# Kernel optimization log

Hardware: AMD Instinct MI355X
Metric: run time of the kernel (lower is better)

## Reference

```python
import jax, jax.numpy as jnp
import numpy as np
import math

B, S, D, H = 2, 2048, 512, 8
DK = D // H  # 64
NEG_INF = float('-inf')


def setup_inputs() -> dict:
    key = jax.random.key(0)
    ks = jax.random.split(key, 16)
    s = 1.0 / math.sqrt(D)
    return {
        'in_Q': jax.random.normal(ks[0], (B, S, D), jnp.float32),
        'in_K': jax.random.normal(ks[1], (B, S, D), jnp.float32),
        'in_V': jax.random.normal(ks[2], (B, S, D), jnp.float32),
        'row_pad_mask': jax.random.randint(ks[3], (B, S), 0, 2, jnp.int32),
        'col_pad_mask': jax.random.randint(ks[4], (B, S), 0, 2, jnp.int32),
        'W_Q': jax.random.uniform(ks[5], (D, D), jnp.float32, -s, s),
        'b_Q': jax.random.uniform(ks[6], (D,), jnp.float32, -s, s),
        'W_K': jax.random.uniform(ks[7], (D, D), jnp.float32, -s, s),
        'b_K': jax.random.uniform(ks[8], (D,), jnp.float32, -s, s),
        'W_V': jax.random.uniform(ks[9], (D, D), jnp.float32, -s, s),
        'b_V': jax.random.uniform(ks[10], (D,), jnp.float32, -s, s),
        'W_O': jax.random.uniform(ks[11], (D, D), jnp.float32, -s, s),
        'b_O': jax.random.uniform(ks[12], (D,), jnp.float32, -s, s),
    }


def reference(in_Q, in_K, in_V, row_pad_mask, col_pad_mask,
              W_Q, b_Q, W_K, b_K, W_V, b_V, W_O, b_O):
    b, sq, _ = in_Q.shape
    sk = in_K.shape[1]
    # projections (torch Linear: x @ W.T + b)
    Q = in_Q @ W_Q.T + b_Q
    K = in_K @ W_K.T + b_K
    V = in_V @ W_V.T + b_V
    # chunk along feature dim + stack == reshape to heads: [b, h, s, dk]
    Qh = Q.reshape(b, sq, H, DK).transpose(0, 2, 1, 3)
    Kh = K.reshape(b, sk, H, DK).transpose(0, 2, 1, 3)
    Vh = V.reshape(b, sk, H, DK).transpose(0, 2, 1, 3)
    scores = jnp.einsum('bhqd,bhkd->bhqk', Qh, Kh) / math.sqrt(DK)
    # causal mask (additive -inf above diagonal, as in the original)
    causal = jnp.triu(jnp.full((sq, sk), NEG_INF, scores.dtype), k=1)
    scores = scores + causal
    # padding masks: pad masks encode lengths via their row sums
    row_len = row_pad_mask.sum(axis=1)  # [b]
    col_len = col_pad_mask.sum(axis=1)
    row_np = jnp.arange(sq)[None, :] < row_len[:, None]  # [b, sq]
    col_np = jnp.arange(sk)[None, :] < col_len[:, None]  # [b, sk]
    non_pad = (row_np[:, :, None] & col_np[:, None, :])[:, None]  # [b,1,sq,sk]
    scores = jnp.where(non_pad, scores, NEG_INF)
    p = jax.nn.softmax(scores, axis=-1)
    p = jnp.nan_to_num(p)  # fully-masked rows -> 0 (matches torch nan_to_num)
    attn = jnp.einsum('bhqk,bhkd->bhqd', p, Vh)
    Hcat = attn.transpose(0, 2, 1, 3).reshape(b, sq, D)
    return Hcat @ W_O.T + b_O
```

## Files before the change

### kernel.cpp

```cpp
#include <hip/hip_runtime.h>

#define S_LEN 2048
#define D_MODEL 512
#define NHEAD 8
#define BATCH 2

typedef __attribute__((ext_vector_type(8))) short bf16x8;
typedef __attribute__((ext_vector_type(4))) float f32x4;

__device__ __forceinline__ unsigned short f2bf(float f) {
    union { float f; unsigned u; } v; v.f = f;
    unsigned u = v.u + 0x7FFFu + ((v.u >> 16) & 1u);
    return (unsigned short)(u >> 16);
}

__device__ __forceinline__ float ex2(float x) {
    return __builtin_amdgcn_exp2f(x);
}

__device__ __forceinline__ unsigned cvtpk(float lo, float hi) {
    unsigned r;
    asm("v_cvt_pk_bf16_f32 %0, %1, %2" : "=v"(r) : "v"(lo), "v"(hi));
    return r;
}

__device__ __forceinline__ void gl_lds16(const unsigned short* g, unsigned short* l) {
    __builtin_amdgcn_global_load_lds(
        (const __attribute__((address_space(1))) void*)g,
        (__attribute__((address_space(3))) void*)l,
        16, 0, 0);
}

__global__ __launch_bounds__(256) void cvtlens_kernel(
    const float* __restrict__ inQ, const float* __restrict__ inK, const float* __restrict__ inV,
    const float* __restrict__ WQ, const float* __restrict__ WK,
    const float* __restrict__ WV, const float* __restrict__ WO,
    const int* __restrict__ rpm, const int* __restrict__ cpm,
    unsigned short* __restrict__ Xbf, unsigned short* __restrict__ Wbf,
    int* __restrict__ lens)
{
    const int t = threadIdx.x;
    if (blockIdx.x < 2) {
        __shared__ int red[256];
        const int b = blockIdx.x;
        int sr = 0, sc2 = 0;
        for (int i = t; i < S_LEN; i += 256) {
            sr  += rpm[b * S_LEN + i];
            sc2 += cpm[b * S_LEN + i];
        }
        red[t] = sr;
        __syncthreads();
        for (int off = 128; off > 0; off >>= 1) {
            if (t < off) red[t] += red[t + off];
            __syncthreads();
        }
        if (t == 0) lens[b * 2 + 0] = red[0];
        __syncthreads();
        red[t] = sc2;
        __syncthreads();
        for (int off = 128; off > 0; off >>= 1) {
            if (t < off) red[t] += red[t + off];
            __syncthreads();
        }
        if (t == 0) lens[b * 2 + 1] = red[0];
    }

    const int NXC = 786432;
    const int NTOT = 917504;
    const int stride = gridDim.x * 256;
    for (int c = blockIdx.x * 256 + t; c < NTOT; c += stride) {
        if (c < NXC) {
            const int flat = c << 3;
            const int z = flat >> 21;
            const int off = flat & 2097151;
            const float* src = ((z == 0) ? inQ : (z == 1) ? inK : inV) + off;
            float4 a = *(const float4*)src;
            float4 d = *(const float4*)(src + 4);
            unsigned short* w = Xbf + flat;
            w[0] = f2bf(a.x); w[1] = f2bf(a.y); w[2] = f2bf(a.z); w[3] = f2bf(a.w);
            w[4] = f2bf(d.x); w[5] = f2bf(d.y); w[6] = f2bf(d.z); w[7] = f2bf(d.w);
        } else {
            const int wflat = (c - NXC) << 3;
            const int wz = wflat >> 18;
            const int off = wflat & 262143;
            const float* src = ((wz == 0) ? WQ : (wz == 1) ? WK : (wz == 2) ? WV : WO) + off;
            float4 a = *(const float4*)src;
            float4 d = *(const float4*)(src + 4);
            unsigned short* w = Wbf + wflat;
            w[0] = f2bf(a.x); w[1] = f2bf(a.y); w[2] = f2bf(a.z); w[3] = f2bf(a.w);
            w[4] = f2bf(d.x); w[5] = f2bf(d.y); w[6] = f2bf(d.z); w[7] = f2bf(d.w);
        }
    }
}

__global__ __launch_bounds__(256) void proj_gemm(
    const unsigned short* __restrict__ Xbf, const unsigned short* __restrict__ Wbf,
    const float* __restrict__ bQ, const float* __restrict__ bK, const float* __restrict__ bV,
    const int* __restrict__ lens,
    unsigned short* __restrict__ Qg, unsigned short* __restrict__ Kg,
    unsigned short* __restrict__ VTg)
{
    __shared__ __align__(16) unsigned short Xld[2][8192];
    __shared__ __align__(16) unsigned short Wld[2][8192];

    const int z = blockIdx.z;
    const int tileS = blockIdx.x * 128;
    const int tileF = blockIdx.y * 128;
    const int bb0 = tileS >> 11;
    const int rl = lens[bb0 * 2], cl = lens[bb0 * 2 + 1];
    const int limit = (z == 0) ? rl : cl;
    if ((tileS & 2047) >= limit) return;

    const unsigned short* X = Xbf + (size_t)z * (4096 * 512);
    const unsigned short* W = Wbf + (size_t)z * (512 * 512);
    const float* bias = (z == 0) ? bQ : (z == 1) ? bK : bV;

    const int t = threadIdx.x;
    const int wv = t >> 6, lane = t & 63, l15 = lane & 15, quad = lane >> 4;
    const int ro = lane >> 3;
    const int lc8 = ((lane & 7) ^ ro) * 8;

    const unsigned short* gX = X + (size_t)(tileS + wv * 32 + ro) * 512 + lc8;
    const unsigned short* gW = W + (size_t)(tileF + wv * 32 + ro) * 512 + lc8;
    const int wvo = wv * 2048;

    const int f_off = (wv & 1) * 64, s_off = (wv >> 1) * 64;
    const int swk = l15 & 7;

    f32x4 acc[4][4] = {};

    #pragma unroll
    for (int j = 0; j < 4; ++j) {
        gl_lds16(gX + j * 4096, &Xld[0][wvo + j * 512]);
        gl_lds16(gW + j * 4096, &Wld[0][wvo + j * 512]);
    }

    for (int kk = 0; kk < 8; ++kk) {
        __syncthreads();
        if (kk < 7) {
            const int k0 = (kk + 1) * 64;
            const int nb = (kk + 1) & 1;
            #pragma unroll
            for (int j = 0; j < 4; ++j) {
                gl_lds16(gX + k0 + j * 4096, &Xld[nb][wvo + j * 512]);
                gl_lds16(gW + k0 + j * 4096, &Wld[nb][wvo + j * 512]);
            }
        }
        const unsigned short* Xb = Xld[kk & 1];
        const unsigned short* Wb = Wld[kk & 1];
        #pragma unroll
        for (int kk2 = 0; kk2 < 2; ++kk2) {
            bf16x8 wf[4], xf[4];
            #pragma unroll
            for (int i = 0; i < 4; ++i) {
                const int rw = f_off + i * 16 + l15;
                wf[i] = *(const bf16x8*)(Wb + rw * 64 + ((kk2 * 4 + quad) ^ swk) * 8);
                const int rx = s_off + i * 16 + l15;
                xf[i] = *(const bf16x8*)(Xb + rx * 64 + ((kk2 * 4 + quad) ^ swk) * 8);
            }
            #pragma unroll
            for (int ft = 0; ft < 4; ++ft)
                #pragma unroll
                for (int st = 0; st < 4; ++st)
                    acc[ft][st] = __builtin_amdgcn_mfma_f32_16x16x32_bf16(
                        wf[ft], xf[st], acc[ft][st], 0, 0, 0);
        }
    }

    const float oscale = (z == 0) ? 0.18033688011112042f : 1.0f;
    #pragma unroll
    for (int ft = 0; ft < 4; ++ft) {
        const int f = tileF + f_off + ft * 16 + quad * 4;
        const int h = f >> 6, dk = f & 63;
        const float b0 = bias[f], b1 = bias[f + 1], b2 = bias[f + 2], b3 = bias[f + 3];
        #pragma unroll
        for (int st = 0; st < 4; ++st) {
            const int s = tileS + s_off + st * 16 + l15;
            const int bb = s >> 11, seq = s & 2047;
            const f32x4 a = acc[ft][st];
            if (z <= 1) {
                unsigned short* dst = ((z == 0) ? Qg : Kg)
                    + ((size_t)((bb * 8 + h) * 2048 + seq)) * 64 + dk;
                ushort4 u;
                u.x = f2bf((a[0] + b0) * oscale); u.y = f2bf((a[1] + b1) * oscale);
                u.z = f2bf((a[2] + b2) * oscale); u.w = f2bf((a[3] + b3) * oscale);
                *(ushort4*)dst = u;
            } else {
                unsigned short* dst = VTg
                    + ((size_t)((bb * 8 + h) * 64 + dk)) * 2048 + seq;
                dst[0]    = f2bf(a[0] + b0);
                dst[2048] = f2bf(a[1] + b1);
                dst[4096] = f2bf(a[2] + b2);
                dst[6144] = f2bf(a[3] + b3);
            }
        }
    }
}

__global__ __launch_bounds__(256) void attn_kernel(
    const unsigned short* __restrict__ Qg, const unsigned short* __restrict__ Kg,
    const unsigned short* __restrict__ VTg, const int* __restrict__ lens,
    unsigned short* __restrict__ AO)
{
    __shared__ __align__(16) char smem[32768 + 512];
    unsigned short* stage = (unsigned short*)smem;
    float* Ml = (float*)(smem + 32768);
    float* Ll = Ml + 64;

    const int t = threadIdx.x;
    const int wv = t >> 6, lane = t & 63, l15 = lane & 15, quad = lane >> 4;
    const int bh = blockIdx.y;
    const int b = bh >> 3, h = bh & 7;
    const int q0 = blockIdx.x * 16;
    const int rl = lens[b * 2], cl = lens[b * 2 + 1];

    if (q0 >= rl) {
        const int row = t >> 4, cg = t & 15;
        ushort4 zz = {0, 0, 0, 0};
        *(ushort4*)(AO + ((size_t)(b * 2048 + q0 + row)) * 512 + h * 64 + cg * 4) = zz;
        return;
    }

    const unsigned short* Qrow = Qg + ((size_t)(bh * 2048 + q0 + l15)) * 64;
    const bf16x8 aq0 = *(const bf16x8*)(Qrow + quad * 8);
    const bf16x8 aq1 = *(const bf16x8*)(Qrow + 32 + quad * 8);

    unsigned short* stw = stage + wv * 4096;

    const int sro = lane >> 3;
    const int c0 = (((lane & 7) ^ (sro & 3)) << 3);
    const int sk = l15 & 7;
    const int sv = (l15 & 3) | ((l15 & 8) >> 1);
    const int skq0 = ((quad ^ sk) << 3), skq1 = (((quad + 4) ^ sk) << 3);
    const int svq0 = ((quad ^ sv) << 3), svq1 = (((quad + 4) ^ sv) << 3);

    f32x4 oacc[4] = {};
    float m_ = -__builtin_inff(), l_ = 0.f;

    const int q_end = q0 + 16;
    const int kv_max = (cl < q_end) ? cl : q_end;
    const int ntiles = (kv_max + 63) >> 6;
    const int qme = q0 + l15;

    for (int kt = wv; kt < ntiles; kt += 4) {
        const int kv0 = kt * 64;

        {
            const unsigned short* kgb = Kg + ((size_t)(bh * 2048 + kv0 + sro)) * 64;
            #pragma unroll
            for (int j = 0; j < 8; ++j)
                gl_lds16(kgb + j * 512 + (c0 ^ ((j & 1) << 5)), stw + j * 512);
        }
        __builtin_amdgcn_s_waitcnt(0x0070);

        f32x4 sc[4];
        __builtin_amdgcn_s_setprio(1);
        #pragma unroll
        for (int ct = 0; ct < 4; ++ct) {
            const int grow = ((l15 >> 2) << 3) + ((ct & 1) << 2) + (l15 & 3)
                           + ((ct >> 1) << 5);
            const unsigned short* krow = stw + grow * 64;
            const bf16x8 kf0 = *(const bf16x8*)(krow + skq0);
            const bf16x8 kf1 = *(const bf16x8*)(krow + skq1);
            f32x4 zz = {};
            zz = __builtin_amdgcn_mfma_f32_16x16x32_bf16(kf0, aq0, zz, 0, 0, 0);
            sc[ct] = __builtin_amdgcn_mfma_f32_16x16x32_bf16(kf1, aq1, zz, 0, 0, 0);
        }
        __builtin_amdgcn_s_setprio(0);
        __builtin_amdgcn_s_waitcnt(0x0070);

        {
            const unsigned short* vgb = VTg + ((size_t)(bh * 64 + sro)) * 2048 + kv0;
            #pragma unroll
            for (int j = 0; j < 8; ++j)
                gl_lds16(vgb + j * 16384 + (c0 ^ ((j & 1) << 5)), stw + j * 512);
        }

        const bool full = (kv0 + 64 <= q0) && (kv0 + 64 <= cl) && (q_end <= rl);
        if (!full) {
            #pragma unroll
            for (int ct = 0; ct < 4; ++ct) {
                const int kvb = kv0 + quad * 8 + ((ct & 1) << 2) + ((ct >> 1) << 5);
                #pragma unroll
                for (int r = 0; r < 4; ++r) {
                    const int kv = kvb + r;
                    const bool valid = (qme < rl) && (kv < cl) && (kv <= qme);
                    sc[ct][r] = valid ? sc[ct][r] : -__builtin_inff();
                }
            }
        }

        float mx = -__builtin_inff();
        #pragma unroll
        for (int ct = 0; ct < 4; ++ct)
            mx = fmaxf(mx, fmaxf(fmaxf(sc[ct][0], sc[ct][1]),
                                 fmaxf(sc[ct][2], sc[ct][3])));
        mx = fmaxf(mx, __shfl_xor(mx, 16));
        mx = fmaxf(mx, __shfl_xor(mx, 32));

        const float mnew = fmaxf(m_, mx);
        const float alpha = (m_ == -__builtin_inff()) ? 0.f : ex2(m_ - mnew);
        const float mden = (mnew == -__builtin_inff()) ? 0.f : mnew;

        float psum = 0.f;
        #pragma unroll
        for (int ct = 0; ct < 4; ++ct) {
            #pragma unroll
            for (int r = 0; r < 4; ++r)
                sc[ct][r] = ex2(sc[ct][r] - mden);
            psum += (sc[ct][0] + sc[ct][1]) + (sc[ct][2] + sc[ct][3]);
        }
        psum += __shfl_xor(psum, 16);
        psum += __shfl_xor(psum, 32);
        l_ = alpha * l_ + psum;
        m_ = mnew;

        const float ar0 = __shfl(alpha, quad * 4 + 0);
        const float ar1 = __shfl(alpha, quad * 4 + 1);
        const float ar2 = __shfl(alpha, quad * 4 + 2);
        const float ar3 = __shfl(alpha, quad * 4 + 3);
        #pragma unroll
        for (int ct = 0; ct < 4; ++ct) {
            oacc[ct][0] *= ar0; oacc[ct][1] *= ar1;
            oacc[ct][2] *= ar2; oacc[ct][3] *= ar3;
        }

        union { bf16x8 v; unsigned u[4]; } P0, P1;
        P0.u[0] = cvtpk(sc[0][0], sc[0][1]);
        P0.u[1] = cvtpk(sc[0][2], sc[0][3]);
        P0.u[2] = cvtpk(sc[1][0], sc[1][1]);
        P0.u[3] = cvtpk(sc[1][2], sc[1][3]);
        P1.u[0] = cvtpk(sc[2][0], sc[2][1]);
        P1.u[1] = cvtpk(sc[2][2], sc[2][3]);
        P1.u[2] = cvtpk(sc[3][0], sc[3][1]);
        P1.u[3] = cvtpk(sc[3][2], sc[3][3]);

        __builtin_amdgcn_s_waitcnt(0x0070);
        __builtin_amdgcn_s_setprio(1);
        #pragma unroll
        for (int ct = 0; ct < 4; ++ct) {
            const unsigned short* vrow = stw + (ct * 16 + l15) * 64;
            const bf16x8 vf0 = *(const bf16x8*)(vrow + svq0);
            const bf16x8 vf1 = *(const bf16x8*)(vrow + svq1);
            oacc[ct] = __builtin_amdgcn_mfma_f32_16x16x32_bf16(P0.v, vf0, oacc[ct], 0, 0, 0);
            oacc[ct] = __builtin_amdgcn_mfma_f32_16x16x32_bf16(P1.v, vf1, oacc[ct], 0, 0, 0);
        }
        __builtin_amdgcn_s_setprio(0);
    }

    if (lane < 16) {
        Ml[wv * 16 + l15] = m_;
        Ll[wv * 16 + l15] = l_;
    }
    __syncthreads();

    float* Po = (float*)smem;
    #pragma unroll
    for (int ct = 0; ct < 4; ++ct) {
        #pragma unroll
        for (int r = 0; r < 4; ++r)
            Po[wv * 1088 + (quad * 4 + r) * 68 + ct * 16 + l15] = oacc[ct][r];
    }
    __syncthreads();

    const int row = t >> 4, cg = t & 15;
    float mw[4];
    float mstar = -__builtin_inff();
    #pragma unroll
    for (int w = 0; w < 4; ++w) {
        mw[w] = Ml[w * 16 + row];
        mstar = fmaxf(mstar, mw[w]);
    }
    f32x4 o = {};
    if (mstar != -__builtin_inff()) {
        float lst = 0.f;
        #pragma unroll
        for (int w = 0; w < 4; ++w) {
            const float sw = (mw[w] == -__builtin_inff()) ? 0.f : ex2(mw[w] - mstar);
            lst += sw * Ll[w * 16 + row];
            const f32x4 pv = *(const f32x4*)&Po[w * 1088 + row * 68 + cg * 4];
            o[0] += sw * pv[0]; o[1] += sw * pv[1];
            o[2] += sw * pv[2]; o[3] += sw * pv[3];
        }
        const float inv = (lst > 0.f) ? 1.f / lst : 0.f;
        o[0] *= inv; o[1] *= inv; o[2] *= inv; o[3] *= inv;
    }
    ushort4 u;
    u.x = f2bf(o[0]); u.y = f2bf(o[1]); u.z = f2bf(o[2]); u.w = f2bf(o[3]);
    *(ushort4*)(AO + ((size_t)(b * 2048 + q0 + row)) * 512 + h * 64 + cg * 4) = u;
}

__global__ __launch_bounds__(256) void out_gemm(
    const unsigned short* __restrict__ AO, const unsigned short* __restrict__ Wbf,
    const float* __restrict__ bO, const int* __restrict__ lens, float* __restrict__ out)
{
    __shared__ __align__(16) unsigned short Xld[2][8192];
    __shared__ __align__(16) unsigned short Wld[2][8192];

    const int tileS = blockIdx.x * 128;
    const int tileF = blockIdx.y * 128;
    const int bb0 = tileS >> 11;
    const int rl = lens[bb0 * 2];
    const int t = threadIdx.x;

    if ((tileS & 2047) >= rl) {
        const int r0 = t >> 2;
        const int cg = (t & 3) * 32;
        float4 bv[8];
        #pragma unroll
        for (int j = 0; j < 8; ++j) bv[j] = *(const float4*)(bO + tileF + cg + j * 4);
        #pragma unroll
        for (int i = 0; i < 2; ++i) {
            float* orow = out + (size_t)(tileS + i * 64 + r0) * 512 + tileF + cg;
            #pragma unroll
            for (int j = 0; j < 8; ++j) *(float4*)(orow + j * 4) = bv[j];
        }
        return;
    }

    const unsigned short* W = Wbf + (size_t)3 * (512 * 512);
    const int wv = t >> 6, lane = t & 63, l15 = lane & 15, quad = lane >> 4;
    const int ro = lane >> 3;
    const int lc8 = ((lane & 7) ^ ro) * 8;

    const unsigned short* gX = AO + (size_t)(tileS + wv * 32 + ro) * 512 + lc8;
    const unsigned short* gW = W + (size_t)(tileF + wv * 32 + ro) * 512 + lc8;
    const int wvo = wv * 2048;

    const int f_off = (wv & 1) * 64, s_off = (wv >> 1) * 64;
    const int swk = l15 & 7;

    f32x4 acc[4][4] = {};

    #pragma unroll
    for (int j = 0; j < 4; ++j) {
        gl_lds16(gX + j * 4096, &Xld[0][wvo + j * 512]);
        gl_lds16(gW + j * 4096, &Wld[0][wvo + j * 512]);
    }

    for (int kk = 0; kk < 8; ++kk) {
        __syncthreads();
        if (kk < 7) {
            const int k0 = (kk + 1) * 64;
            const int nb = (kk + 1) & 1;
            #pragma unroll
            for (int j = 0; j < 4; ++j) {
                gl_lds16(gX + k0 + j * 4096, &Xld[nb][wvo + j * 512]);
                gl_lds16(gW + k0 + j * 4096, &Wld[nb][wvo + j * 512]);
            }
        }
        const unsigned short* Xb = Xld[kk & 1];
        const unsigned short* Wb = Wld[kk & 1];
        #pragma unroll
        for (int kk2 = 0; kk2 < 2; ++kk2) {
            bf16x8 wf[4], xf[4];
            #pragma unroll
            for (int i = 0; i < 4; ++i) {
                const int rw = f_off + i * 16 + l15;
                wf[i] = *(const bf16x8*)(Wb + rw * 64 + ((kk2 * 4 + quad) ^ swk) * 8);
                const int rx = s_off + i * 16 + l15;
                xf[i] = *(const bf16x8*)(Xb + rx * 64 + ((kk2 * 4 + quad) ^ swk) * 8);
            }
            #pragma unroll
            for (int ft = 0; ft < 4; ++ft)
                #pragma unroll
                for (int st = 0; st < 4; ++st)
                    acc[ft][st] = __builtin_amdgcn_mfma_f32_16x16x32_bf16(
                        wf[ft], xf[st], acc[ft][st], 0, 0, 0);
        }
    }

    #pragma unroll
    for (int ft = 0; ft < 4; ++ft) {
        const int f = tileF + f_off + ft * 16 + quad * 4;
        const float4 bv = *(const float4*)(bO + f);
        #pragma unroll
        for (int st = 0; st < 4; ++st) {
            const int s = tileS + s_off + st * 16 + l15;
            float4 o;
            o.x = acc[ft][st][0] + bv.x;
            o.y = acc[ft][st][1] + bv.y;
            o.z = acc[ft][st][2] + bv.z;
            o.w = acc[ft][st][3] + bv.w;
            *(float4*)(out + (size_t)s * 512 + f) = o;
        }
    }
}

extern "C" void kernel_launch(void* const* d_in, const int* in_sizes, int n_in,
                              void* d_out, int out_size, void* d_ws, size_t ws_size,
                              hipStream_t stream)
{
    const float* inQ = (const float*)d_in[0];
    const float* inK = (const float*)d_in[1];
    const float* inV = (const float*)d_in[2];
    const int*   rpm = (const int*)d_in[3];
    const int*   cpm = (const int*)d_in[4];
    const float* WQ  = (const float*)d_in[5];
    const float* bQ  = (const float*)d_in[6];
    const float* WK  = (const float*)d_in[7];
    const float* bK  = (const float*)d_in[8];
    const float* WV  = (const float*)d_in[9];
    const float* bV  = (const float*)d_in[10];
    const float* WO  = (const float*)d_in[11];
    const float* bO  = (const float*)d_in[12];
    float* out = (float*)d_out;

    char* ws = (char*)d_ws;
    unsigned short* Xbf = (unsigned short*)(ws);
    unsigned short* Wbf = (unsigned short*)(ws + 12582912);
    unsigned short* Qg  = (unsigned short*)(ws + 14680064);
    unsigned short* Kg  = (unsigned short*)(ws + 18874368);
    unsigned short* VTg = (unsigned short*)(ws + 23068672);
    unsigned short* AO  = (unsigned short*)(ws + 27262976);
    int* lens           = (int*)(ws + 31457280);

    cvtlens_kernel<<<dim3(1792), dim3(256), 0, stream>>>(
        inQ, inK, inV, WQ, WK, WV, WO, rpm, cpm, Xbf, Wbf, lens);
    proj_gemm<<<dim3(32, 4, 3), dim3(256), 0, stream>>>(
        Xbf, Wbf, bQ, bK, bV, lens, Qg, Kg, VTg);
    attn_kernel<<<dim3(128, 16), dim3(256), 0, stream>>>(Qg, Kg, VTg, lens, AO);
    out_gemm<<<dim3(32, 4), dim3(256), 0, stream>>>(AO, Wbf, bO, lens, out);
}
```

Before: 143.8 us.

## Process 32 query rows per attention block to reuse staged K/V tiles

Each attention block now covers two 16-row query subtiles instead of one. Every K and V tile loaded into LDS feeds MFMAs for both subtiles, and the grid is halved. This cuts redundant K/V global loads and per-block overhead. The cost is more accumulator registers, a larger Po reduction buffer, and coarser causal load balance, since fewer blocks each do more work.

```diff
diff --git a/kernel.cpp b/kernel.cpp
--- a/kernel.cpp
+++ b/kernel.cpp
@@ -202,28 +202,35 @@
     const unsigned short* __restrict__ VTg, const int* __restrict__ lens,
     unsigned short* __restrict__ AO)
 {
-    __shared__ __align__(16) char smem[32768 + 512];
+    __shared__ __align__(16) char smem[35840];
     unsigned short* stage = (unsigned short*)smem;
-    float* Ml = (float*)(smem + 32768);
-    float* Ll = Ml + 64;
+    float* Ml = (float*)(smem + 34816);
+    float* Ll = Ml + 128;
 
     const int t = threadIdx.x;
     const int wv = t >> 6, lane = t & 63, l15 = lane & 15, quad = lane >> 4;
     const int bh = blockIdx.y;
     const int b = bh >> 3, h = bh & 7;
-    const int q0 = blockIdx.x * 16;
+    const int q0 = blockIdx.x * 32;
     const int rl = lens[b * 2], cl = lens[b * 2 + 1];
 
     if (q0 >= rl) {
         const int row = t >> 4, cg = t & 15;
         ushort4 zz = {0, 0, 0, 0};
-        *(ushort4*)(AO + ((size_t)(b * 2048 + q0 + row)) * 512 + h * 64 + cg * 4) = zz;
+        #pragma unroll
+        for (int rr = 0; rr < 2; ++rr)
+            *(ushort4*)(AO + ((size_t)(b * 2048 + q0 + rr * 16 + row)) * 512
+                        + h * 64 + cg * 4) = zz;
         return;
     }
 
-    const unsigned short* Qrow = Qg + ((size_t)(bh * 2048 + q0 + l15)) * 64;
-    const bf16x8 aq0 = *(const bf16x8*)(Qrow + quad * 8);
-    const bf16x8 aq1 = *(const bf16x8*)(Qrow + 32 + quad * 8);
+    bf16x8 aq[2][2];
+    #pragma unroll
+    for (int qs = 0; qs < 2; ++qs) {
+        const unsigned short* Qrow = Qg + ((size_t)(bh * 2048 + q0 + qs * 16 + l15)) * 64;
+        aq[qs][0] = *(const bf16x8*)(Qrow + quad * 8);
+        aq[qs][1] = *(const bf16x8*)(Qrow + 32 + quad * 8);
+    }
 
     unsigned short* stw = stage + wv * 4096;
 
@@ -234,13 +241,14 @@
     const int skq0 = ((quad ^ sk) << 3), skq1 = (((quad + 4) ^ sk) << 3);
     const int svq0 = ((quad ^ sv) << 3), svq1 = (((quad + 4) ^ sv) << 3);
 
-    f32x4 oacc[4] = {};
-    float m_ = -__builtin_inff(), l_ = 0.f;
-
-    const int q_end = q0 + 16;
+    f32x4 oacc[2][4] = {};
+    float m_[2], l_[2];
+    #pragma unroll
+    for (int qs = 0; qs < 2; ++qs) { m_[qs] = -__builtin_inff(); l_[qs] = 0.f; }
+
+    const int q_end = q0 + 32;
     const int kv_max = (cl < q_end) ? cl : q_end;
     const int ntiles = (kv_max + 63) >> 6;
-    const int qme = q0 + l15;
 
     for (int kt = wv; kt < ntiles; kt += 4) {
         const int kv0 = kt * 64;
@@ -253,7 +261,7 @@
         }
         __builtin_amdgcn_s_waitcnt(0x0070);
 
-        f32x4 sc[4];
+        f32x4 sc[2][4];
         __builtin_amdgcn_s_setprio(1);
         #pragma unroll
         for (int ct = 0; ct < 4; ++ct) {
@@ -262,9 +270,12 @@
             const unsigned short* krow = stw + grow * 64;
             const bf16x8 kf0 = *(const bf16x8*)(krow + skq0);
             const bf16x8 kf1 = *(const bf16x8*)(krow + skq1);
-            f32x4 zz = {};
-            zz = __builtin_amdgcn_mfma_f32_16x16x32_bf16(kf0, aq0, zz, 0, 0, 0);
-            sc[ct] = __builtin_amdgcn_mfma_f32_16x16x32_bf16(kf1, aq1, zz, 0, 0, 0);
+            #pragma unroll
+            for (int qs = 0; qs < 2; ++qs) {
+                f32x4 zz = {};
+                zz = __builtin_amdgcn_mfma_f32_16x16x32_bf16(kf0, aq[qs][0], zz, 0, 0, 0);
+                sc[qs][ct] = __builtin_amdgcn_mfma_f32_16x16x32_bf16(kf1, aq[qs][1], zz, 0, 0, 0);
+            }
         }
         __builtin_amdgcn_s_setprio(0);
         __builtin_amdgcn_s_waitcnt(0x0070);
@@ -277,63 +288,68 @@
         }
 
         const bool full = (kv0 + 64 <= q0) && (kv0 + 64 <= cl) && (q_end <= rl);
-        if (!full) {
+
+        union { bf16x8 v; unsigned u[4]; } P0[2], P1[2];
+        #pragma unroll
+        for (int qs = 0; qs < 2; ++qs) {
+            const int qme = q0 + qs * 16 + l15;
+            if (!full) {
+                #pragma unroll
+                for (int ct = 0; ct < 4; ++ct) {
+                    const int kvb = kv0 + quad * 8 + ((ct & 1) << 2) + ((ct >> 1) << 5);
+                    #pragma unroll
+                    for (int r = 0; r < 4; ++r) {
+                        const int kv = kvb + r;
+                        const bool valid = (qme < rl) && (kv < cl) && (kv <= qme);
+                        sc[qs][ct][r] = valid ? sc[qs][ct][r] : -__builtin_inff();
+                    }
+                }
+            }
+
+            float mx = -__builtin_inff();
+            #pragma unroll
+            for (int ct = 0; ct < 4; ++ct)
+                mx = fmaxf(mx, fmaxf(fmaxf(sc[qs][ct][0], sc[qs][ct][1]),
+                                     fmaxf(sc[qs][ct][2], sc[qs][ct][3])));
+            mx = fmaxf(mx, __shfl_xor(mx, 16));
+            mx = fmaxf(mx, __shfl_xor(mx, 32));
+
+            const float mnew = fmaxf(m_[qs], mx);
+            const float alpha = (m_[qs] == -__builtin_inff()) ? 0.f : ex2(m_[qs] - mnew);
+            const float mden = (mnew == -__builtin_inff()) ? 0.f : mnew;
+
+            float psum = 0.f;
             #pragma unroll
             for (int ct = 0; ct < 4; ++ct) {
-                const int kvb = kv0 + quad * 8 + ((ct & 1) << 2) + ((ct >> 1) << 5);
                 #pragma unroll
-                for (int r = 0; r < 4; ++r) {
-                    const int kv = kvb + r;
-                    const bool valid = (qme < rl) && (kv < cl) && (kv <= qme);
-                    sc[ct][r] = valid ? sc[ct][r] : -__builtin_inff();
-                }
-            }
-        }
-
-        float mx = -__builtin_inff();
-        #pragma unroll
-        for (int ct = 0; ct < 4; ++ct)
-            mx = fmaxf(mx, fmaxf(fmaxf(sc[ct][0], sc[ct][1]),
-                                 fmaxf(sc[ct][2], sc[ct][3])));
-        mx = fmaxf(mx, __shfl_xor(mx, 16));
-        mx = fmaxf(mx, __shfl_xor(mx, 32));
-
-        const float mnew = fmaxf(m_, mx);
-        const float alpha = (m_ == -__builtin_inff()) ? 0.f : ex2(m_ - mnew);
-        const float mden = (mnew == -__builtin_inff()) ? 0.f : mnew;
-
-        float psum = 0.f;
-        #pragma unroll
-        for (int ct = 0; ct < 4; ++ct) {
-            #pragma unroll
-            for (int r = 0; r < 4; ++r)
-                sc[ct][r] = ex2(sc[ct][r] - mden);
-            psum += (sc[ct][0] + sc[ct][1]) + (sc[ct][2] + sc[ct][3]);
-        }
-        psum += __shfl_xor(psum, 16);
-        psum += __shfl_xor(psum, 32);
-        l_ = alpha * l_ + psum;
-        m_ = mnew;
-
-        const float ar0 = __shfl(alpha, quad * 4 + 0);
-        const float ar1 = __shfl(alpha, quad * 4 + 1);
-        const float ar2 = __shfl(alpha, quad * 4 + 2);
-        const float ar3 = __shfl(alpha, quad * 4 + 3);
-        #pragma unroll
-        for (int ct = 0; ct < 4; ++ct) {
-            oacc[ct][0] *= ar0; oacc[ct][1] *= ar1;
-            oacc[ct][2] *= ar2; oacc[ct][3] *= ar3;
-        }
-
-        union { bf16x8 v; unsigned u[4]; } P0, P1;
-        P0.u[0] = cvtpk(sc[0][0], sc[0][1]);
-        P0.u[1] = cvtpk(sc[0][2], sc[0][3]);
-        P0.u[2] = cvtpk(sc[1][0], sc[1][1]);
-        P0.u[3] = cvtpk(sc[1][2], sc[1][3]);
-        P1.u[0] = cvtpk(sc[2][0], sc[2][1]);
-        P1.u[1] = cvtpk(sc[2][2], sc[2][3]);
-        P1.u[2] = cvtpk(sc[3][0], sc[3][1]);
-        P1.u[3] = cvtpk(sc[3][2], sc[3][3]);
+                for (int r = 0; r < 4; ++r)
+                    sc[qs][ct][r] = ex2(sc[qs][ct][r] - mden);
+                psum += (sc[qs][ct][0] + sc[qs][ct][1]) + (sc[qs][ct][2] + sc[qs][ct][3]);
+            }
+            psum += __shfl_xor(psum, 16);
+            psum += __shfl_xor(psum, 32);
+            l_[qs] = alpha * l_[qs] + psum;
+            m_[qs] = mnew;
+
+            const float ar0 = __shfl(alpha, quad * 4 + 0);
+            const float ar1 = __shfl(alpha, quad * 4 + 1);
+            const float ar2 = __shfl(alpha, quad * 4 + 2);
+            const float ar3 = __shfl(alpha, quad * 4 + 3);
+            #pragma unroll
+            for (int ct = 0; ct < 4; ++ct) {
+                oacc[qs][ct][0] *= ar0; oacc[qs][ct][1] *= ar1;
+                oacc[qs][ct][2] *= ar2; oacc[qs][ct][3] *= ar3;
+            }
+
+            P0[qs].u[0] = cvtpk(sc[qs][0][0], sc[qs][0][1]);
+            P0[qs].u[1] = cvtpk(sc[qs][0][2], sc[qs][0][3]);
+            P0[qs].u[2] = cvtpk(sc[qs][1][0], sc[qs][1][1]);
+            P0[qs].u[3] = cvtpk(sc[qs][1][2], sc[qs][1][3]);
+            P1[qs].u[0] = cvtpk(sc[qs][2][0], sc[qs][2][1]);
+            P1[qs].u[1] = cvtpk(sc[qs][2][2], sc[qs][2][3]);
+            P1[qs].u[2] = cvtpk(sc[qs][3][0], sc[qs][3][1]);
+            P1[qs].u[3] = cvtpk(sc[qs][3][2], sc[qs][3][3]);
+        }
 
         __builtin_amdgcn_s_waitcnt(0x0070);
         __builtin_amdgcn_s_setprio(1);
@@ -342,52 +358,63 @@
             const unsigned short* vrow = stw + (ct * 16 + l15) * 64;
             const bf16x8 vf0 = *(const bf16x8*)(vrow + svq0);
             const bf16x8 vf1 = *(const bf16x8*)(vrow + svq1);
-            oacc[ct] = __builtin_amdgcn_mfma_f32_16x16x32_bf16(P0.v, vf0, oacc[ct], 0, 0, 0);
-            oacc[ct] = __builtin_amdgcn_mfma_f32_16x16x32_bf16(P1.v, vf1, oacc[ct], 0, 0, 0);
+            #pragma unroll
+            for (int qs = 0; qs < 2; ++qs) {
+                oacc[qs][ct] = __builtin_amdgcn_mfma_f32_16x16x32_bf16(P0[qs].v, vf0, oacc[qs][ct], 0, 0, 0);
+                oacc[qs][ct] = __builtin_amdgcn_mfma_f32_16x16x32_bf16(P1[qs].v, vf1, oacc[qs][ct], 0, 0, 0);
+            }
         }
         __builtin_amdgcn_s_setprio(0);
     }
 
     if (lane < 16) {
-        Ml[wv * 16 + l15] = m_;
-        Ll[wv * 16 + l15] = l_;
+        #pragma unroll
+        for (int qs = 0; qs < 2; ++qs) {
+            Ml[wv * 32 + qs * 16 + l15] = m_[qs];
+            Ll[wv * 32 + qs * 16 + l15] = l_[qs];
+        }
     }
     __syncthreads();
 
     float* Po = (float*)smem;
     #pragma unroll
-    for (int ct = 0; ct < 4; ++ct) {
-        #pragma unroll
-        for (int r = 0; r < 4; ++r)
-            Po[wv * 1088 + (quad * 4 + r) * 68 + ct * 16 + l15] = oacc[ct][r];
-    }
+    for (int qs = 0; qs < 2; ++qs)
+        #pragma unroll
+        for (int ct = 0; ct < 4; ++ct)
+            #pragma unroll
+            for (int r = 0; r < 4; ++r)
+                Po[wv * 2176 + (qs * 16 + quad * 4 + r) * 68 + ct * 16 + l15] = oacc[qs][ct][r];
     __syncthreads();
 
     const int row = t >> 4, cg = t & 15;
-    float mw[4];
-    float mstar = -__builtin_inff();
-    #pragma unroll
-    for (int w = 0; w < 4; ++w) {
-        mw[w] = Ml[w * 16 + row];
-        mstar = fmaxf(mstar, mw[w]);
-    }
-    f32x4 o = {};
-    if (mstar != -__builtin_inff()) {
-        float lst = 0.f;
+    #pragma unroll
+    for (int rr = 0; rr < 2; ++rr) {
+        const int orow = rr * 16 + row;
+        float mw[4];
+        float mstar = -__builtin_inff();
         #pragma unroll
         for (int w = 0; w < 4; ++w) {
-            const float sw = (mw[w] == -__builtin_inff()) ? 0.f : ex2(mw[w] - mstar);
-            lst += sw * Ll[w * 16 + row];
-            const f32x4 pv = *(const f32x4*)&Po[w * 1088 + row * 68 + cg * 4];
-            o[0] += sw * pv[0]; o[1] += sw * pv[1];
-            o[2] += sw * pv[2]; o[3] += sw * pv[3];
-        }
-        const float inv = (lst > 0.f) ? 1.f / lst : 0.f;
-        o[0] *= inv; o[1] *= inv; o[2] *= inv; o[3] *= inv;
-    }
-    ushort4 u;
-    u.x = f2bf(o[0]); u.y = f2bf(o[1]); u.z = f2bf(o[2]); u.w = f2bf(o[3]);
-    *(ushort4*)(AO + ((size_t)(b * 2048 + q0 + row)) * 512 + h * 64 + cg * 4) = u;
+            mw[w] = Ml[w * 32 + orow];
+            mstar = fmaxf(mstar, mw[w]);
+        }
+        f32x4 o = {};
+        if (mstar != -__builtin_inff()) {
+            float lst = 0.f;
+            #pragma unroll
+            for (int w = 0; w < 4; ++w) {
+                const float sw = (mw[w] == -__builtin_inff()) ? 0.f : ex2(mw[w] - mstar);
+                lst += sw * Ll[w * 32 + orow];
+                const f32x4 pv = *(const f32x4*)&Po[w * 2176 + orow * 68 + cg * 4];
+                o[0] += sw * pv[0]; o[1] += sw * pv[1];
+                o[2] += sw * pv[2]; o[3] += sw * pv[3];
+            }
+            const float inv = (lst > 0.f) ? 1.f / lst : 0.f;
+            o[0] *= inv; o[1] *= inv; o[2] *= inv; o[3] *= inv;
+        }
+        ushort4 u;
+        u.x = f2bf(o[0]); u.y = f2bf(o[1]); u.z = f2bf(o[2]); u.w = f2bf(o[3]);
+        *(ushort4*)(AO + ((size_t)(b * 2048 + q0 + orow)) * 512 + h * 64 + cg * 4) = u;
+    }
 }
 
 __global__ __launch_bounds__(256) void out_gemm(
@@ -519,6 +546,6 @@
         inQ, inK, inV, WQ, WK, WV, WO, rpm, cpm, Xbf, Wbf, lens);
     proj_gemm<<<dim3(32, 4, 3), dim3(256), 0, stream>>>(
         Xbf, Wbf, bQ, bK, bV, lens, Qg, Kg, VTg);
-    attn_kernel<<<dim3(128, 16), dim3(256), 0, stream>>>(Qg, Kg, VTg, lens, AO);
+    attn_kernel<<<dim3(64, 16), dim3(256), 0, stream>>>(Qg, Kg, VTg, lens, AO);
     out_gemm<<<dim3(32, 4), dim3(256), 0, stream>>>(AO, Wbf, bO, lens, out);
 }
```

After: 141.3 us. No clear change (-1.7%).
